# Kernel tuning notes

Measured on AMD Instinct MI355X. Metric: run time of the kernel, lower is better.

Reference implementation:

```python
import jax, jax.numpy as jnp
import numpy as np

B = 16384
IN_DIM = 28 * 28
HID = 768
NUM_EXPERTS = 8
NUM_CLASSES = 10
H_PHASOR = 32          # phasor bank harmonics -> 2*H features
DELTA0 = 7.0
DECAY = 0.7            # spiking attention leak
THETA = 1.0
K_WINNERS = 5
TOP_K_ROUTE = 2
TRAITS = (0.6, 0.6, 0.5, 0.5, 0.4)


def setup_inputs() -> dict:
    key = jax.random.key(0)
    ks = jax.random.split(key, 16)
    s = 0.02
    return {
        "x": jax.random.normal(ks[0], (B, 28, 28), jnp.float32),
        "W_in": jax.random.normal(ks[1], (IN_DIM, HID), jnp.float32) * s,
        "b_in": jnp.zeros((HID,), jnp.float32),
        "W_ph": jax.random.normal(ks[2], (2 * H_PHASOR, HID), jnp.float32) * s,
        "b_ph": jnp.zeros((HID,), jnp.float32),
        "W_gate": jax.random.normal(ks[3], (HID, NUM_EXPERTS), jnp.float32) * s,
        "b_gate": jnp.zeros((NUM_EXPERTS,), jnp.float32),
        "W_exp": jax.random.normal(ks[4], (NUM_EXPERTS, HID, HID), jnp.float32) * s,
        "b_exp": jnp.zeros((NUM_EXPERTS, HID), jnp.float32),
        "W_th": jax.random.normal(ks[5], (HID, NUM_EXPERTS), jnp.float32) * s,
        "b_th": jnp.zeros((NUM_EXPERTS,), jnp.float32),
        "W_pm": jax.random.normal(ks[6], (5, NUM_EXPERTS), jnp.float32) * s,
        "b_pm": jnp.zeros((NUM_EXPERTS,), jnp.float32),
        "W_out": jax.random.normal(ks[7], (HID, NUM_CLASSES), jnp.float32) * s,
        "b_out": jnp.zeros((NUM_CLASSES,), jnp.float32),
    }


def reference(x, W_in, b_in, W_ph, b_ph, W_gate, b_gate, W_exp, b_exp,
              W_th, b_th, W_pm, b_pm, W_out, b_out):
    Bn = x.shape[0]
    x_flat = x.reshape((Bn, -1))
    proj = x_flat @ W_in + b_in                                  # [B, HID]

    # Phasor bank on per-sample mean activation: sin/cos at H harmonics
    x_mean = jnp.mean(proj, axis=-1)                             # [B]
    freqs = DELTA0 * jnp.arange(1, H_PHASOR + 1, dtype=proj.dtype)
    phase = x_mean[:, None] * freqs[None, :]                     # [B, H]
    feats = jnp.concatenate([jnp.sin(phase), jnp.cos(phase)], -1)  # [B, 2H]
    enhanced = proj + feats @ W_ph + b_ph                        # [B, HID]

    # Top-K index selection feeding gather/scatter spiking attention
    V = enhanced.shape[-1]
    K = min(32, V)
    topk_idx = jax.lax.top_k(enhanced, K)[1].astype(jnp.int32)   # [B, K]
    w = DECAY ** jnp.arange(K, dtype=enhanced.dtype)             # decaying drive

    def gains_fn(idx):
        v = jnp.zeros((V,), enhanced.dtype).at[idx].add(w)       # scatter-add
        vals, widx = jax.lax.top_k(v, K_WINNERS)                 # k-WTA
        return jnp.ones((V,), enhanced.dtype).at[widx].add(vals / THETA)

    gains = jax.vmap(gains_fn)(topk_idx)                         # [B, V]
    attended = enhanced * gains

    # Personality bias + thalamic bias (thalamic_scale = 1.0)
    traits = jnp.asarray(TRAITS, dtype=enhanced.dtype)
    pbias = traits @ W_pm + b_pm                                 # [E]
    thal = jnp.mean(attended, axis=0) @ W_th + b_th              # [E]

    # MoE retrieval core: gate -> top-k softmax route -> combine experts
    gate_logits = attended @ W_gate + b_gate + pbias[None] + thal[None]  # [B, E]
    gvals, gidx = jax.lax.top_k(gate_logits, TOP_K_ROUTE)        # [B, k]
    gw = jax.nn.softmax(gvals, axis=-1)                          # [B, k]
    exp_out = jnp.einsum('bh,ehd->bed', attended, W_exp) + b_exp[None]   # [B, E, HID]
    sel = jnp.take_along_axis(exp_out, gidx[:, :, None], axis=1)  # [B, k, HID]
    context = jnp.sum(gw[:, :, None] * sel, axis=1)              # [B, HID]

    return context @ W_out + b_out                               # [B, classes]
```

## Files before the change

### kernel.cpp

```cpp
#include <hip/hip_runtime.h>
#include <hip/hip_bf16.h>
#include <cstddef>

#define BATCH 16384
#define IND   784
#define HID   768
#define NEXP  8
#define KT13  13

typedef short bf16x8 __attribute__((ext_vector_type(8)));
typedef float f32x4  __attribute__((ext_vector_type(4)));
typedef unsigned short ushort_t;

#define GLD16(g, l)                                                            \
  __builtin_amdgcn_global_load_lds(                                            \
      (const __attribute__((address_space(1))) unsigned int*)(g),              \
      (__attribute__((address_space(3))) unsigned int*)(l), 16, 0, 0)

__global__ __launch_bounds__(256) void k_wtrans(const float* __restrict__ Wexp,
                                                __hip_bfloat16* __restrict__ Wt)
{
  __shared__ float tile[32][33];
  const int e = blockIdx.z;
  const int h0 = blockIdx.x * 32, d0 = blockIdx.y * 32;
  const int tx = threadIdx.x & 31, ty = threadIdx.x >> 5;
  const float* src = Wexp + ((size_t)e * HID + h0) * HID + d0;
  #pragma unroll
  for (int i = 0; i < 4; i++)
    tile[ty + 8 * i][tx] = src[(size_t)(ty + 8 * i) * HID + tx];
  __syncthreads();
  __hip_bfloat16* dst = Wt + ((size_t)e * HID + d0) * HID + h0;
  #pragma unroll
  for (int i = 0; i < 4; i++)
    dst[(size_t)(ty + 8 * i) * HID + tx] = __float2bfloat16(tile[tx][ty + 8 * i]);
}

__device__ inline ushort_t bf16_rne(float f) {
  union { float f; unsigned u; } v; v.f = f;
  unsigned r = v.u + 0x7fffu + ((v.u >> 16) & 1u);
  return (ushort_t)(r >> 16);
}
__device__ inline float bf16_to_f(ushort_t h) {
  union { unsigned u; float f; } v; v.u = ((unsigned)h) << 16;
  return v.f;
}

__global__ __launch_bounds__(256) void k_packA(const float* __restrict__ x,
                                               ushort_t* __restrict__ Ahi,
                                               ushort_t* __restrict__ Alo)
{
  const int kt = blockIdx.x, mt = blockIdx.y;
  const size_t tbase = ((size_t)mt * KT13 + kt) * 8192;
  const int kb = kt * 64;
  #pragma unroll
  for (int i = 0; i < 4; i++) {
    int id = i * 256 + threadIdx.x;
    int r = id >> 3, c = id & 7;
    int row = mt * 128 + r;
    int k0 = kb + c * 8;
    float v[8];
    if (k0 + 8 <= IND) {
      const float4* p = reinterpret_cast<const float4*>(x + (size_t)row * IND + k0);
      float4 a = p[0], b = p[1];
      v[0] = a.x; v[1] = a.y; v[2] = a.z; v[3] = a.w;
      v[4] = b.x; v[5] = b.y; v[6] = b.z; v[7] = b.w;
    } else {
      #pragma unroll
      for (int j = 0; j < 8; j++) v[j] = (k0 + j < IND) ? x[(size_t)row * IND + k0 + j] : 0.f;
    }
    ushort_t hi[8], lo[8];
    #pragma unroll
    for (int j = 0; j < 8; j++) {
      hi[j] = bf16_rne(v[j]);
      lo[j] = bf16_rne(v[j] - bf16_to_f(hi[j]));
    }
    size_t dst = tbase + (size_t)r * 64 + ((c ^ (r & 7)) * 8);
    *reinterpret_cast<uint4*>(Ahi + dst) = *reinterpret_cast<uint4*>(hi);
    *reinterpret_cast<uint4*>(Alo + dst) = *reinterpret_cast<uint4*>(lo);
  }
}

__global__ __launch_bounds__(256) void k_packB(const float* __restrict__ W,
                                               ushort_t* __restrict__ Bhi,
                                               ushort_t* __restrict__ Blo)
{
  const int kt = blockIdx.x, nt = blockIdx.y;
  const size_t tbase = ((size_t)nt * KT13 + kt) * 8192;
  const int kb = kt * 64;
  #pragma unroll
  for (int i = 0; i < 4; i++) {
    int id = i * 256 + threadIdx.x;
    int r = id >> 3, c = id & 7;
    int n = nt * 128 + r;
    int k0 = kb + c * 8;
    float v[8];
    #pragma unroll
    for (int j = 0; j < 8; j++)
      v[j] = (k0 + j < IND) ? W[(size_t)(k0 + j) * HID + n] : 0.f;
    ushort_t hi[8], lo[8];
    #pragma unroll
    for (int j = 0; j < 8; j++) {
      hi[j] = bf16_rne(v[j]);
      lo[j] = bf16_rne(v[j] - bf16_to_f(hi[j]));
    }
    size_t dst = tbase + (size_t)r * 64 + ((c ^ (r & 7)) * 8);
    *reinterpret_cast<uint4*>(Bhi + dst) = *reinterpret_cast<uint4*>(hi);
    *reinterpret_cast<uint4*>(Blo + dst) = *reinterpret_cast<uint4*>(lo);
  }
}

__global__ __launch_bounds__(256, 2) void k_proj2(const ushort_t* __restrict__ Ahi,
                                                  const ushort_t* __restrict__ Alo,
                                                  const ushort_t* __restrict__ Bhi,
                                                  const ushort_t* __restrict__ Blo,
                                                  const float* __restrict__ bias,
                                                  float* __restrict__ out)
{
  __shared__ __align__(16) ushort_t lds[4 * 8192];
  const int tid = threadIdx.x, lane = tid & 63, w = tid >> 6;
  const int mt = blockIdx.y, nt = blockIdx.x;
  const int m0 = (w >> 1) * 64, n0 = (w & 1) * 64;
  const int l15 = lane & 15, g = lane >> 4;

  f32x4 acc[4][4];
  #pragma unroll
  for (int i = 0; i < 4; i++)
    #pragma unroll
    for (int j = 0; j < 4; j++) acc[i][j] = (f32x4){0.f, 0.f, 0.f, 0.f};

  const size_t abase = (size_t)mt * KT13 * 8192;
  const size_t bbase = (size_t)nt * KT13 * 8192;

  for (int kt = 0; kt < KT13; kt++) {
    __syncthreads();
    const ushort_t* srcs[4] = { Ahi + abase + (size_t)kt * 8192,
                                Alo + abase + (size_t)kt * 8192,
                                Bhi + bbase + (size_t)kt * 8192,
                                Blo + bbase + (size_t)kt * 8192 };
    #pragma unroll
    for (int buf = 0; buf < 4; buf++) {
      #pragma unroll
      for (int i = 0; i < 4; i++) {
        int off = w * 2048 + i * 512 + lane * 8;
        GLD16(srcs[buf] + off, &lds[buf * 8192 + w * 2048 + i * 512]);
      }
    }
    asm volatile("s_waitcnt vmcnt(0)");
    __syncthreads();
    #pragma unroll
    for (int ks = 0; ks < 2; ks++) {
      bf16x8 ah[4], al[4], bh[4], bl[4];
      #pragma unroll
      for (int i = 0; i < 4; i++) {
        int ca = ((4 * ks + g) ^ (l15 & 7)) * 8;
        int ra = m0 + 16 * i + l15;
        ah[i] = *reinterpret_cast<const bf16x8*>(&lds[0 * 8192 + ra * 64 + ca]);
        al[i] = *reinterpret_cast<const bf16x8*>(&lds[1 * 8192 + ra * 64 + ca]);
        int rb = n0 + 16 * i + l15;
        bh[i] = *reinterpret_cast<const bf16x8*>(&lds[2 * 8192 + rb * 64 + ca]);
        bl[i] = *reinterpret_cast<const bf16x8*>(&lds[3 * 8192 + rb * 64 + ca]);
      }
      #pragma unroll
      for (int i = 0; i < 4; i++)
        #pragma unroll
        for (int j = 0; j < 4; j++) {
          acc[i][j] = __builtin_amdgcn_mfma_f32_16x16x32_bf16(ah[i], bh[j], acc[i][j], 0, 0, 0);
          acc[i][j] = __builtin_amdgcn_mfma_f32_16x16x32_bf16(ah[i], bl[j], acc[i][j], 0, 0, 0);
          acc[i][j] = __builtin_amdgcn_mfma_f32_16x16x32_bf16(al[i], bh[j], acc[i][j], 0, 0, 0);
        }
    }
  }
  #pragma unroll
  for (int i = 0; i < 4; i++) {
    #pragma unroll
    for (int q = 0; q < 4; q++) {
      int m = mt * 128 + m0 + 16 * i + g * 4 + q;
      #pragma unroll
      for (int j = 0; j < 4; j++) {
        int n = nt * 128 + n0 + 16 * j + l15;
        out[(size_t)m * HID + n] = acc[i][j][q] + bias[n];
      }
    }
  }
}

__global__ __launch_bounds__(256) void k_mean(const float* __restrict__ proj,
                                              float* __restrict__ means)
{
  const int t = threadIdx.x, lane = t & 63, w = t >> 6;
  const int row = blockIdx.x * 4 + w;
  const float* p = proj + (size_t)row * HID;
  float s = 0.f;
  #pragma unroll
  for (int j = 0; j < 12; j++) s += p[lane + 64 * j];
  #pragma unroll
  for (int off = 32; off; off >>= 1) s += __shfl_xor(s, off);
  if (lane == 0) means[row] = s * (1.0f / 768.0f);
}

__global__ __launch_bounds__(256) void k_phasor(const float* __restrict__ means,
                                                const float* __restrict__ Wph,
                                                const float* __restrict__ bph,
                                                float* __restrict__ enh)
{
  __shared__ float Fs[64][132];
  __shared__ float Ws[64][128];
  const int t  = threadIdx.x;
  const int bm = blockIdx.y * 128, bn = blockIdx.x * 128;
  {
    const int r = t >> 1;
    const float mn = means[bm + r];
    if ((t & 1) == 0) {
      #pragma unroll
      for (int j = 0; j < 32; j++) Fs[j][r] = sinf(mn * (7.0f * (j + 1)));
    } else {
      #pragma unroll
      for (int j = 0; j < 32; j++) Fs[32 + j][r] = cosf(mn * (7.0f * (j + 1)));
    }
  }
  #pragma unroll
  for (int i = 0; i < 8; i++) {
    int f4 = i * 256 + t;
    int k = f4 >> 5, n4 = (f4 & 31) * 4;
    *reinterpret_cast<float4*>(&Ws[k][n4]) =
        *reinterpret_cast<const float4*>(Wph + (size_t)k * HID + bn + n4);
  }
  __syncthreads();

  const int m0 = (t >> 4) * 8, n0 = (t & 15) * 8;
  float acc[8][8];
  #pragma unroll
  for (int i = 0; i < 8; i++)
    #pragma unroll
    for (int j = 0; j < 8; j++) acc[i][j] = 0.f;
  #pragma unroll 4
  for (int k = 0; k < 64; k++) {
    float a[8], b[8];
    *reinterpret_cast<float4*>(&a[0]) = *reinterpret_cast<const float4*>(&Fs[k][m0]);
    *reinterpret_cast<float4*>(&a[4]) = *reinterpret_cast<const float4*>(&Fs[k][m0 + 4]);
    *reinterpret_cast<float4*>(&b[0]) = *reinterpret_cast<const float4*>(&Ws[k][n0]);
    *reinterpret_cast<float4*>(&b[4]) = *reinterpret_cast<const float4*>(&Ws[k][n0 + 4]);
    #pragma unroll
    for (int i = 0; i < 8; i++)
      #pragma unroll
      for (int j = 0; j < 8; j++) acc[i][j] = fmaf(a[i], b[j], acc[i][j]);
  }
  float bl[8];
  #pragma unroll
  for (int j = 0; j < 8; j++) bl[j] = bph[bn + n0 + j];
  #pragma unroll
  for (int i = 0; i < 8; i++) {
    float* rowp = enh + (size_t)(bm + m0 + i) * HID + bn + n0;
    float4 p0 = *reinterpret_cast<float4*>(rowp);
    float4 p1 = *reinterpret_cast<float4*>(rowp + 4);
    p0.x += acc[i][0] + bl[0]; p0.y += acc[i][1] + bl[1];
    p0.z += acc[i][2] + bl[2]; p0.w += acc[i][3] + bl[3];
    p1.x += acc[i][4] + bl[4]; p1.y += acc[i][5] + bl[5];
    p1.z += acc[i][6] + bl[6]; p1.w += acc[i][7] + bl[7];
    *reinterpret_cast<float4*>(rowp)     = p0;
    *reinterpret_cast<float4*>(rowp + 4) = p1;
  }
}

__global__ __launch_bounds__(256) void k_attend(const float* __restrict__ enh,
                                                const float* __restrict__ Wg,
                                                __hip_bfloat16* __restrict__ attb,
                                                float* __restrict__ glog,
                                                float* __restrict__ partials)
{
  __shared__ float WgT[8][768];
  __shared__ float cs[4][768];
  const int t = threadIdx.x, lane = t & 63, w = t >> 6;
  for (int i = t; i < 768 * 8; i += 256) { int c = i >> 3, e = i & 7; WgT[e][c] = Wg[i]; }
  for (int i = t; i < 4 * 768; i += 256) cs[i / 768][i % 768] = 0.f;
  __syncthreads();

  for (int rr = 0; rr < 8; ++rr) {
    const int row = blockIdx.x * 32 + rr * 4 + w;
    const float* er = enh + (size_t)row * HID;
    float o[12], s[12];
    #pragma unroll
    for (int j = 0; j < 12; j++) { o[j] = er[lane + 64 * j]; s[j] = o[j]; }

    int wc[5];
    #pragma unroll
    for (int k = 0; k < 5; k++) {
      float v = -3.4e38f; int c = 0x7fffffff;
      #pragma unroll
      for (int j = 0; j < 12; j++)
        if (s[j] > v) { v = s[j]; c = lane + 64 * j; }
      #pragma unroll
      for (int off = 32; off; off >>= 1) {
        float ov = __shfl_xor(v, off); int oc = __shfl_xor(c, off);
        if (ov > v || (ov == v && oc < c)) { v = ov; c = oc; }
      }
      wc[k] = c;
      if (lane == (c & 63)) {
        #pragma unroll
        for (int j = 0; j < 12; j++) if (j == (c >> 6)) s[j] = -3.4e38f;
      }
    }

    float a[12];
    #pragma unroll
    for (int j = 0; j < 12; j++) a[j] = o[j];
    float wv = 1.0f;
    #pragma unroll
    for (int k = 0; k < 5; k++) {
      int c = wc[k];
      if (lane == (c & 63)) {
        #pragma unroll
        for (int j = 0; j < 12; j++) if (j == (c >> 6)) a[j] = o[j] * (1.0f + wv);
      }
      wv *= 0.7f;
    }
    #pragma unroll
    for (int j = 0; j < 12; j++)
      attb[(size_t)row * HID + lane + 64 * j] = __float2bfloat16(a[j]);
    #pragma unroll
    for (int j = 0; j < 12; j++) cs[w][lane + 64 * j] += a[j];

    float p[8];
    #pragma unroll
    for (int e = 0; e < 8; e++) p[e] = 0.f;
    #pragma unroll
    for (int j = 0; j < 12; j++) {
      int c = lane + 64 * j;
      #pragma unroll
      for (int e = 0; e < 8; e++) p[e] = fmaf(a[j], WgT[e][c], p[e]);
    }
    #pragma unroll
    for (int e = 0; e < 8; e++) {
      #pragma unroll
      for (int off = 32; off; off >>= 1) p[e] += __shfl_xor(p[e], off);
    }
    if (lane == 0) {
      #pragma unroll
      for (int e = 0; e < 8; e++) glog[(size_t)row * 8 + e] = p[e];
    }
  }
  __syncthreads();
  for (int i = t; i < 768; i += 256)
    partials[(size_t)blockIdx.x * 768 + i] = cs[0][i] + cs[1][i] + cs[2][i] + cs[3][i];
}

__global__ void k_thal(const float* __restrict__ partials,
                       const float* __restrict__ Wth, const float* __restrict__ bth,
                       const float* __restrict__ Wpm, const float* __restrict__ bpm,
                       const float* __restrict__ bgate, float* __restrict__ add8)
{
  __shared__ float cm[768];
  __shared__ float th[8];
  const int t = threadIdx.x;
  float s = 0.f;
  #pragma unroll 8
  for (int b = 0; b < 512; b++) s += partials[(size_t)b * 768 + t];
  cm[t] = s * (1.0f / 16384.0f);
  __syncthreads();
  if (t < 256) {
    int e = t >> 5, l = t & 31;
    float ps = 0.f;
    for (int c = l; c < 768; c += 32) ps = fmaf(cm[c], Wth[(size_t)c * 8 + e], ps);
    #pragma unroll
    for (int off = 16; off; off >>= 1) ps += __shfl_xor(ps, off);
    if (l == 0) th[e] = ps + bth[e];
  }
  __syncthreads();
  if (t < 8) {
    const float TR[5] = {0.6f, 0.6f, 0.5f, 0.5f, 0.4f};
    float pb = bpm[t];
    #pragma unroll
    for (int i = 0; i < 5; i++) pb = fmaf(TR[i], Wpm[i * 8 + t], pb);
    add8[t] = th[t] + pb + bgate[t];
  }
}

__global__ __launch_bounds__(256) void k_route(const float* __restrict__ glog,
                                               const float* __restrict__ add8,
                                               float* __restrict__ rw,
                                               unsigned char* __restrict__ re,
                                               int* __restrict__ counts)
{
  __shared__ float a8[8];
  __shared__ int lc[8];
  const int t = threadIdx.x;
  if (t < 8) { a8[t] = add8[t]; lc[t] = 0; }
  __syncthreads();
  const int row = blockIdx.x * 256 + t;
  const float4* gp = reinterpret_cast<const float4*>(glog + (size_t)row * 8);
  float4 g0 = gp[0], g1 = gp[1];
  float l[8] = { g0.x + a8[0], g0.y + a8[1], g0.z + a8[2], g0.w + a8[3],
                 g1.x + a8[4], g1.y + a8[5], g1.z + a8[6], g1.w + a8[7] };
  float v0 = l[0], v1 = -3.4e38f; int i0 = 0, i1 = 0;
  #pragma unroll
  for (int e = 1; e < 8; e++) {
    if (l[e] > v0)      { v1 = v0; i1 = i0; v0 = l[e]; i0 = e; }
    else if (l[e] > v1) { v1 = l[e]; i1 = e; }
  }
  float ex = expf(v1 - v0);
  float inv = 1.0f / (1.0f + ex);
  rw[row * 2] = inv; rw[row * 2 + 1] = ex * inv;
  re[row * 2] = (unsigned char)i0; re[row * 2 + 1] = (unsigned char)i1;
  atomicAdd(&lc[i0], 1); atomicAdd(&lc[i1], 1);
  __syncthreads();
  if (t < 8) atomicAdd(&counts[t], lc[t]);
}

__global__ void k_prefix(const int* __restrict__ counts, int* __restrict__ meta)
{
  if (threadIdx.x == 0) {
    int o = 0, tt = 0;
    for (int e = 0; e < 8; e++) {
      meta[e] = o; meta[9 + e] = tt; meta[19 + e] = o;
      o += counts[e]; tt += (counts[e] + 127) >> 7;
    }
    meta[8] = o; meta[17] = tt; meta[18] = tt;
  }
}

__global__ __launch_bounds__(256) void k_scatter(const unsigned char* __restrict__ re,
                                                 int* __restrict__ meta,
                                                 int* __restrict__ perm)
{
  __shared__ int lc[8], base[8];
  const int t = threadIdx.x;
  if (t < 8) lc[t] = 0;
  __syncthreads();
  const int row = blockIdx.x * 256 + t;
  const int e0 = re[row * 2], e1 = re[row * 2 + 1];
  const int p0 = atomicAdd(&lc[e0], 1);
  const int p1 = atomicAdd(&lc[e1], 1);
  __syncthreads();
  if (t < 8) base[t] = atomicAdd(&meta[19 + t], lc[t]);
  __syncthreads();
  perm[base[e0] + p0] = row * 2;
  perm[base[e1] + p1] = row * 2 + 1;
}

__global__ __launch_bounds__(256) void k_expert(const unsigned short* __restrict__ attb,
                                                const unsigned short* __restrict__ Wt,
                                                const float* __restrict__ bexp,
                                                const float* __restrict__ rw,
                                                const int* __restrict__ perm,
                                                const int* __restrict__ meta,
                                                float* __restrict__ s0,
                                                float* __restrict__ s1)
{
  if ((int)blockIdx.x >= meta[18]) return;
  __shared__ unsigned short As[128 * 64];
  __shared__ unsigned short Bs[128 * 64];
  __shared__ int rid[128];
  __shared__ float gws[128];
  __shared__ unsigned char kbit[128];
  __shared__ float bxs[128];

  const int* tst = meta + 9;
  const int tb = blockIdx.x;
  int e = 0;
  #pragma unroll
  for (int i = 1; i < 8; i++) if (tb >= tst[i]) e = i;
  const int tix  = tb - tst[e];
  const int off  = meta[e];
  const int cnt  = meta[e + 1] - off;
  const int rbase = off + tix * 128;
  const int vcnt  = min(128, cnt - tix * 128);
  const int tid = threadIdx.x;
  const int nb  = blockIdx.y * 128;

  if (tid < 128) {
    if (tid < vcnt) {
      int p = perm[rbase + tid];
      rid[tid] = p >> 1; kbit[tid] = p & 1; gws[tid] = rw[p];
    } else {
      rid[tid] = 0; kbit[tid] = 0; gws[tid] = 0.f;
    }
    bxs[tid] = bexp[(size_t)e * HID + nb + tid];
  }
  __syncthreads();

  const int lane = tid & 63, w = tid >> 6;
  const int m0 = (w >> 1) * 64, n0 = (w & 1) * 64;
  const int l15 = lane & 15, g = lane >> 4;

  f32x4 acc[4][4];
  #pragma unroll
  for (int i = 0; i < 4; i++)
    #pragma unroll
    for (int j = 0; j < 4; j++) acc[i][j] = (f32x4){0.f, 0.f, 0.f, 0.f};

  for (int kb = 0; kb < HID; kb += 64) {
    __syncthreads();
    #pragma unroll
    for (int i = 0; i < 4; i++) {
      int id = i * 256 + tid;
      int r = id >> 3, c = id & 7;
      uint4 va = *(reinterpret_cast<const uint4*>(attb + (size_t)rid[r] * HID + kb) + c);
      *reinterpret_cast<uint4*>(As + r * 64 + ((c ^ (r & 7)) * 8)) = va;
      uint4 vb = *(reinterpret_cast<const uint4*>(Wt + ((size_t)e * HID + nb + r) * HID + kb) + c);
      *reinterpret_cast<uint4*>(Bs + r * 64 + ((c ^ (r & 7)) * 8)) = vb;
    }
    __syncthreads();
    #pragma unroll
    for (int ks = 0; ks < 2; ks++) {
      bf16x8 af[4], bfr[4];
      #pragma unroll
      for (int i = 0; i < 4; i++) {
        int r  = m0 + 16 * i + l15;
        af[i]  = *reinterpret_cast<const bf16x8*>(As + r * 64 + (((4 * ks + g) ^ (l15 & 7)) * 8));
        int rn = n0 + 16 * i + l15;
        bfr[i] = *reinterpret_cast<const bf16x8*>(Bs + rn * 64 + (((4 * ks + g) ^ (l15 & 7)) * 8));
      }
      #pragma unroll
      for (int i = 0; i < 4; i++)
        #pragma unroll
        for (int j = 0; j < 4; j++)
          acc[i][j] = __builtin_amdgcn_mfma_f32_16x16x32_bf16(af[i], bfr[j], acc[i][j], 0, 0, 0);
    }
  }
  #pragma unroll
  for (int i = 0; i < 4; i++) {
    #pragma unroll
    for (int q = 0; q < 4; q++) {
      int m = m0 + 16 * i + g * 4 + q;
      if (m < vcnt) {
        int grow = rid[m];
        float gwv = gws[m];
        float* dst = kbit[m] ? s1 : s0;
        #pragma unroll
        for (int j = 0; j < 4; j++) {
          int n = n0 + 16 * j + l15;
          dst[(size_t)grow * HID + nb + n] = gwv * (acc[i][j][q] + bxs[n]);
        }
      }
    }
  }
}

__global__ __launch_bounds__(256) void k_out(const float* __restrict__ s0,
                                             const float* __restrict__ s1,
                                             const float* __restrict__ Wout,
                                             const float* __restrict__ bout,
                                             float* __restrict__ out)
{
  __shared__ float wT[10][768];
  const int t = threadIdx.x, lane = t & 63, w = t >> 6;
  for (int i = t; i < 7680; i += 256) { int cl = i / 768, d = i - cl * 768; wT[cl][d] = Wout[(size_t)d * 10 + cl]; }
  __syncthreads();
  for (int rr = 0; rr < 8; ++rr) {
    const int row = blockIdx.x * 32 + rr * 4 + w;
    const float* a0 = s0 + (size_t)row * HID;
    const float* a1 = s1 + (size_t)row * HID;
    float cd[12];
    #pragma unroll
    for (int j = 0; j < 12; j++) cd[j] = a0[lane + 64 * j] + a1[lane + 64 * j];
    float p[10];
    #pragma unroll
    for (int cl = 0; cl < 10; cl++) {
      float ps = 0.f;
      #pragma unroll
      for (int j = 0; j < 12; j++) ps = fmaf(cd[j], wT[cl][lane + 64 * j], ps);
      #pragma unroll
      for (int off = 32; off; off >>= 1) ps += __shfl_xor(ps, off);
      p[cl] = ps;
    }
    if (lane == 0) {
      #pragma unroll
      for (int cl = 0; cl < 10; cl++) out[(size_t)row * 10 + cl] = p[cl] + bout[cl];
    }
  }
}

extern "C" void kernel_launch(void* const* d_in, const int* in_sizes, int n_in,
                              void* d_out, int out_size, void* d_ws, size_t ws_size,
                              hipStream_t stream)
{
  const float* x     = (const float*)d_in[0];
  const float* W_in  = (const float*)d_in[1];
  const float* b_in  = (const float*)d_in[2];
  const float* W_ph  = (const float*)d_in[3];
  const float* b_ph  = (const float*)d_in[4];
  const float* W_g   = (const float*)d_in[5];
  const float* b_g   = (const float*)d_in[6];
  const float* W_exp = (const float*)d_in[7];
  const float* b_exp = (const float*)d_in[8];
  const float* W_th  = (const float*)d_in[9];
  const float* b_th  = (const float*)d_in[10];
  const float* W_pm  = (const float*)d_in[11];
  const float* b_pm  = (const float*)d_in[12];
  const float* W_out = (const float*)d_in[13];
  const float* b_out = (const float*)d_in[14];
  float* out = (float*)d_out;

  char* ws = (char*)d_ws;
  size_t off = 0;
  float* enh   = (float*)(ws + off); off += (size_t)BATCH * HID * 4;
  char*  aliasbase = ws + off;
  float* slot1 = (float*)(ws + off); off += (size_t)BATCH * HID * 4;
  __hip_bfloat16* attb = (__hip_bfloat16*)(ws + off); off += (size_t)BATCH * HID * 2;
  __hip_bfloat16* Wt   = (__hip_bfloat16*)(ws + off); off += (size_t)NEXP * HID * HID * 2;
  float* glog     = (float*)(ws + off); off += (size_t)BATCH * 8 * 4;
  float* partials = (float*)(ws + off); off += (size_t)512 * 768 * 4;
  float* means    = (float*)(ws + off); off += (size_t)BATCH * 4;
  float* add8     = (float*)(ws + off); off += 256;
  float* rw       = (float*)(ws + off); off += (size_t)BATCH * 2 * 4;
  unsigned char* re = (unsigned char*)(ws + off); off += (size_t)BATCH * 2;
  int* counts = (int*)(ws + off); off += 256;
  int* meta   = (int*)(ws + off); off += 256;
  int* perm   = (int*)(ws + off); off += (size_t)BATCH * 2 * 4;
  ushort_t* Bhi = (ushort_t*)(ws + off); off += (size_t)KT13 * 64 * HID * 2;
  ushort_t* Blo = (ushort_t*)(ws + off); off += (size_t)KT13 * 64 * HID * 2;
  ushort_t* Ahi = (ushort_t*)aliasbase;
  ushort_t* Alo = (ushort_t*)(aliasbase + (size_t)BATCH * KT13 * 64 * 2);

  hipMemsetAsync(counts, 0, 32, stream);
  k_wtrans<<<dim3(24, 24, 8), 256, 0, stream>>>(W_exp, Wt);
  k_packA <<<dim3(13, 128),   256, 0, stream>>>(x, Ahi, Alo);
  k_packB <<<dim3(13, 6),     256, 0, stream>>>(W_in, Bhi, Blo);
  k_proj2 <<<dim3(6, 128),    256, 0, stream>>>(Ahi, Alo, Bhi, Blo, b_in, enh);
  k_mean  <<<4096,            256, 0, stream>>>(enh, means);
  k_phasor<<<dim3(6, 128),    256, 0, stream>>>(means, W_ph, b_ph, enh);
  k_attend<<<512,             256, 0, stream>>>(enh, W_g, attb, glog, partials);
  k_thal  <<<1,               768, 0, stream>>>(partials, W_th, b_th, W_pm, b_pm, b_g, add8);
  k_route <<<64,              256, 0, stream>>>(glog, add8, rw, re, counts);
  k_prefix<<<1,                64, 0, stream>>>(counts, meta);
  k_scatter<<<64,             256, 0, stream>>>(re, meta, perm);
  k_expert<<<dim3(264, 6),    256, 0, stream>>>((const unsigned short*)attb, (const unsigned short*)Wt,
                                                b_exp, rw, perm, meta, enh, slot1);
  k_out   <<<512,             256, 0, stream>>>(enh, slot1, W_out, b_out, out);
}
```

Before: 344.4 us.

## Register-prefetch expert GEMM tiles and store per-slot contexts in bf16

The expert GEMM now prefetches the next K-tile from global memory into registers while MFMAs run on the current LDS tile. This hides load latency behind compute. The two per-slot context buffers are written as bf16 instead of fp32, which halves the expert epilogue writes and the k_out reads. k_out also switches to a contiguous per-lane chunk layout with a row-major W_out in LDS. Storing contexts in bf16 adds rounding error before the final projection, and the prefetch raises register pressure.

```diff
diff --git a/kernel.cpp b/kernel.cpp
--- a/kernel.cpp
+++ b/kernel.cpp
@@ -9,6 +9,7 @@
 #define KT13  13
 
 typedef short bf16x8 __attribute__((ext_vector_type(8)));
+typedef short bf16x4 __attribute__((ext_vector_type(4)));
 typedef float f32x4  __attribute__((ext_vector_type(4)));
 typedef unsigned short ushort_t;
 
@@ -443,8 +444,8 @@
                                                 const float* __restrict__ rw,
                                                 const int* __restrict__ perm,
                                                 const int* __restrict__ meta,
-                                                float* __restrict__ s0,
-                                                float* __restrict__ s1)
+                                                ushort_t* __restrict__ s0,
+                                                ushort_t* __restrict__ s1)
 {
   if ((int)blockIdx.x >= meta[18]) return;
   __shared__ unsigned short As[128 * 64];
@@ -481,6 +482,9 @@
   const int lane = tid & 63, w = tid >> 6;
   const int m0 = (w >> 1) * 64, n0 = (w & 1) * 64;
   const int l15 = lane & 15, g = lane >> 4;
+  const int cr = tid >> 3, cc = tid & 7;
+  const int swz = ((cc ^ (cr & 7)) * 8);
+  const unsigned short* wbase = Wt + ((size_t)e * HID + nb) * HID;
 
   f32x4 acc[4][4];
   #pragma unroll
@@ -488,35 +492,59 @@
     #pragma unroll
     for (int j = 0; j < 4; j++) acc[i][j] = (f32x4){0.f, 0.f, 0.f, 0.f};
 
-  for (int kb = 0; kb < HID; kb += 64) {
+#define LOADT(kb, ra, rb)                                                               \
+  {                                                                                     \
+    _Pragma("unroll")                                                                   \
+    for (int i = 0; i < 4; i++) {                                                       \
+      ra[i] = *(reinterpret_cast<const uint4*>(attb + (size_t)rid[cr + 32 * i] * HID + (kb)) + cc); \
+      rb[i] = *(reinterpret_cast<const uint4*>(wbase + (size_t)(cr + 32 * i) * HID + (kb)) + cc);   \
+    }                                                                                   \
+  }
+#define STORET(ra, rb)                                                                  \
+  {                                                                                     \
+    _Pragma("unroll")                                                                   \
+    for (int i = 0; i < 4; i++) {                                                       \
+      *reinterpret_cast<uint4*>(As + (cr + 32 * i) * 64 + swz) = ra[i];                 \
+      *reinterpret_cast<uint4*>(Bs + (cr + 32 * i) * 64 + swz) = rb[i];                 \
+    }                                                                                   \
+  }
+#define MFMA_STEP()                                                                     \
+  {                                                                                     \
+    _Pragma("unroll")                                                                   \
+    for (int ks = 0; ks < 2; ks++) {                                                    \
+      bf16x8 af[4], bfr[4];                                                             \
+      _Pragma("unroll")                                                                 \
+      for (int i = 0; i < 4; i++) {                                                     \
+        int ca = (((4 * ks + g) ^ (l15 & 7)) * 8);                                      \
+        af[i]  = *reinterpret_cast<const bf16x8*>(As + (m0 + 16 * i + l15) * 64 + ca);  \
+        bfr[i] = *reinterpret_cast<const bf16x8*>(Bs + (n0 + 16 * i + l15) * 64 + ca);  \
+      }                                                                                 \
+      _Pragma("unroll")                                                                 \
+      for (int i = 0; i < 4; i++)                                                       \
+        _Pragma("unroll")                                                               \
+        for (int j = 0; j < 4; j++)                                                     \
+          acc[i][j] = __builtin_amdgcn_mfma_f32_16x16x32_bf16(af[i], bfr[j], acc[i][j], 0, 0, 0); \
+    }                                                                                   \
+  }
+
+  uint4 a0[4], b0[4], a1[4], b1[4];
+  LOADT(0, a0, b0);
+  for (int kb = 0; kb < HID; kb += 128) {
     __syncthreads();
-    #pragma unroll
-    for (int i = 0; i < 4; i++) {
-      int id = i * 256 + tid;
-      int r = id >> 3, c = id & 7;
-      uint4 va = *(reinterpret_cast<const uint4*>(attb + (size_t)rid[r] * HID + kb) + c);
-      *reinterpret_cast<uint4*>(As + r * 64 + ((c ^ (r & 7)) * 8)) = va;
-      uint4 vb = *(reinterpret_cast<const uint4*>(Wt + ((size_t)e * HID + nb + r) * HID + kb) + c);
-      *reinterpret_cast<uint4*>(Bs + r * 64 + ((c ^ (r & 7)) * 8)) = vb;
-    }
+    STORET(a0, b0);
     __syncthreads();
-    #pragma unroll
-    for (int ks = 0; ks < 2; ks++) {
-      bf16x8 af[4], bfr[4];
-      #pragma unroll
-      for (int i = 0; i < 4; i++) {
-        int r  = m0 + 16 * i + l15;
-        af[i]  = *reinterpret_cast<const bf16x8*>(As + r * 64 + (((4 * ks + g) ^ (l15 & 7)) * 8));
-        int rn = n0 + 16 * i + l15;
-        bfr[i] = *reinterpret_cast<const bf16x8*>(Bs + rn * 64 + (((4 * ks + g) ^ (l15 & 7)) * 8));
-      }
-      #pragma unroll
-      for (int i = 0; i < 4; i++)
-        #pragma unroll
-        for (int j = 0; j < 4; j++)
-          acc[i][j] = __builtin_amdgcn_mfma_f32_16x16x32_bf16(af[i], bfr[j], acc[i][j], 0, 0, 0);
-    }
-  }
+    LOADT(kb + 64, a1, b1);
+    MFMA_STEP();
+    __syncthreads();
+    STORET(a1, b1);
+    __syncthreads();
+    if (kb + 128 < HID) LOADT(kb + 128, a0, b0);
+    MFMA_STEP();
+  }
+#undef LOADT
+#undef STORET
+#undef MFMA_STEP
+
   #pragma unroll
   for (int i = 0; i < 4; i++) {
     #pragma unroll
@@ -525,43 +553,55 @@
       if (m < vcnt) {
         int grow = rid[m];
         float gwv = gws[m];
-        float* dst = kbit[m] ? s1 : s0;
+        ushort_t* dst = kbit[m] ? s1 : s0;
         #pragma unroll
         for (int j = 0; j < 4; j++) {
           int n = n0 + 16 * j + l15;
-          dst[(size_t)grow * HID + nb + n] = gwv * (acc[i][j][q] + bxs[n]);
+          dst[(size_t)grow * HID + nb + n] = bf16_rne(gwv * (acc[i][j][q] + bxs[n]));
         }
       }
     }
   }
 }
 
-__global__ __launch_bounds__(256) void k_out(const float* __restrict__ s0,
-                                             const float* __restrict__ s1,
+__global__ __launch_bounds__(256) void k_out(const ushort_t* __restrict__ s0,
+                                             const ushort_t* __restrict__ s1,
                                              const float* __restrict__ Wout,
                                              const float* __restrict__ bout,
                                              float* __restrict__ out)
 {
-  __shared__ float wT[10][768];
+  __shared__ float wTT[768][10];
   const int t = threadIdx.x, lane = t & 63, w = t >> 6;
-  for (int i = t; i < 7680; i += 256) { int cl = i / 768, d = i - cl * 768; wT[cl][d] = Wout[(size_t)d * 10 + cl]; }
-  __syncthreads();
+  for (int i = t; i < 7680; i += 256) ((float*)wTT)[i] = Wout[i];
+  __syncthreads();
+  const int base = lane * 12;
   for (int rr = 0; rr < 8; ++rr) {
     const int row = blockIdx.x * 32 + rr * 4 + w;
-    const float* a0 = s0 + (size_t)row * HID;
-    const float* a1 = s1 + (size_t)row * HID;
+    const ushort_t* p0 = s0 + (size_t)row * HID + base;
+    const ushort_t* p1 = s1 + (size_t)row * HID + base;
+    bf16x8 v0a = *reinterpret_cast<const bf16x8*>(p0);
+    bf16x4 v0b = *reinterpret_cast<const bf16x4*>(p0 + 8);
+    bf16x8 v1a = *reinterpret_cast<const bf16x8*>(p1);
+    bf16x4 v1b = *reinterpret_cast<const bf16x4*>(p1 + 8);
     float cd[12];
     #pragma unroll
-    for (int j = 0; j < 12; j++) cd[j] = a0[lane + 64 * j] + a1[lane + 64 * j];
+    for (int j = 0; j < 8; j++)
+      cd[j] = bf16_to_f((ushort_t)v0a[j]) + bf16_to_f((ushort_t)v1a[j]);
+    #pragma unroll
+    for (int j = 0; j < 4; j++)
+      cd[8 + j] = bf16_to_f((ushort_t)v0b[j]) + bf16_to_f((ushort_t)v1b[j]);
     float p[10];
     #pragma unroll
+    for (int cl = 0; cl < 10; cl++) p[cl] = 0.f;
+    #pragma unroll
+    for (int j = 0; j < 12; j++) {
+      #pragma unroll
+      for (int cl = 0; cl < 10; cl++) p[cl] = fmaf(cd[j], wTT[base + j][cl], p[cl]);
+    }
+    #pragma unroll
     for (int cl = 0; cl < 10; cl++) {
-      float ps = 0.f;
-      #pragma unroll
-      for (int j = 0; j < 12; j++) ps = fmaf(cd[j], wT[cl][lane + 64 * j], ps);
-      #pragma unroll
-      for (int off = 32; off; off >>= 1) ps += __shfl_xor(ps, off);
-      p[cl] = ps;
+      #pragma unroll
+      for (int off = 32; off; off >>= 1) p[cl] += __shfl_xor(p[cl], off);
     }
     if (lane == 0) {
       #pragma unroll
@@ -595,7 +635,7 @@
   size_t off = 0;
   float* enh   = (float*)(ws + off); off += (size_t)BATCH * HID * 4;
   char*  aliasbase = ws + off;
-  float* slot1 = (float*)(ws + off); off += (size_t)BATCH * HID * 4;
+  off += (size_t)BATCH * HID * 4;
   __hip_bfloat16* attb = (__hip_bfloat16*)(ws + off); off += (size_t)BATCH * HID * 2;
   __hip_bfloat16* Wt   = (__hip_bfloat16*)(ws + off); off += (size_t)NEXP * HID * HID * 2;
   float* glog     = (float*)(ws + off); off += (size_t)BATCH * 8 * 4;
@@ -611,6 +651,8 @@
   ushort_t* Blo = (ushort_t*)(ws + off); off += (size_t)KT13 * 64 * HID * 2;
   ushort_t* Ahi = (ushort_t*)aliasbase;
   ushort_t* Alo = (ushort_t*)(aliasbase + (size_t)BATCH * KT13 * 64 * 2);
+  ushort_t* ctx0 = (ushort_t*)enh;
+  ushort_t* ctx1 = ctx0 + (size_t)BATCH * HID;
 
   hipMemsetAsync(counts, 0, 32, stream);
   k_wtrans<<<dim3(24, 24, 8), 256, 0, stream>>>(W_exp, Wt);
@@ -625,6 +667,6 @@
   k_prefix<<<1,                64, 0, stream>>>(counts, meta);
   k_scatter<<<64,             256, 0, stream>>>(re, meta, perm);
   k_expert<<<dim3(264, 6),    256, 0, stream>>>((const unsigned short*)attb, (const unsigned short*)Wt,
-                                                b_exp, rw, perm, meta, enh, slot1);
-  k_out   <<<512,             256, 0, stream>>>(enh, slot1, W_out, b_out, out);
-}
+                                                b_exp, rw, perm, meta, ctx0, ctx1);
+  k_out   <<<512,             256, 0, stream>>>(ctx0, ctx1, W_out, b_out, out);
+}
```

Result: slower. 492.8 us (+43.1%).
